# Performance work log

Measured on AMD Instinct MI355X. Metric: run time of the kernel, lower is better.

The kernel has to match this reference:

```python
import jax, jax.numpy as jnp
import numpy as np

B, T, D, H = 32, 512, 512, 512  # batch, seq_len, emb dim, lstm_size
TAGS = (17, 9, 25, 13)


def _reverse_sequence(x, lengths):
    # tf.reverse_sequence semantics: reverse first `len` steps, keep the tail.
    t = jnp.arange(x.shape[1])
    idx = jnp.where(t[None, :] < lengths[:, None], lengths[:, None] - 1 - t[None, :], t[None, :])
    return jnp.take_along_axis(x, idx[:, :, None], axis=1)


def _lstm(x, W, b, lengths):
    # TF LSTMCell: kernel [D+H,4H], gate order (i, j, f, o), forget_bias=1.0.
    # dynamic_rnn: state copied through past seq_len, outputs zeroed past seq_len.
    Bx, Tx, _ = x.shape
    Hh = b.shape[-1] // 4
    xT = jnp.swapaxes(x, 0, 1)  # [T,B,D]
    mask = (jnp.arange(Tx)[:, None] < lengths[None, :]).astype(x.dtype)[:, :, None]  # [T,B,1]

    def step(carry, inp):
        c, h = carry
        xt, m = inp
        z = jnp.concatenate([xt, h], axis=-1) @ W + b  # [B,4H]
        i, j, f, o = jnp.split(z, 4, axis=-1)
        c_new = jax.nn.sigmoid(f + 1.0) * c + jax.nn.sigmoid(i) * jnp.tanh(j)
        h_new = jax.nn.sigmoid(o) * jnp.tanh(c_new)
        c = m * c_new + (1.0 - m) * c
        h = m * h_new + (1.0 - m) * h
        return (c, h), h * m

    init = (jnp.zeros((Bx, Hh), x.dtype), jnp.zeros((Bx, Hh), x.dtype))
    _, hs = jax.lax.scan(step, init, (xT, mask))
    return jnp.swapaxes(hs, 0, 1)  # [B,T,H]


def _bilstm(x, lengths, Wf, bf, Wb, bb):
    out_fw = _lstm(x, Wf, bf, lengths)
    x_rev = _reverse_sequence(x, lengths)
    out_bw = _reverse_sequence(_lstm(x_rev, Wb, bb, lengths), lengths)
    return jnp.concatenate([out_fw, out_bw], axis=2)  # [B,T,2H]


def setup_inputs() -> dict:
    key = jax.random.key(0)
    ks = jax.random.split(key, 12)
    s_in = 1.0 / np.sqrt(D + H)
    s_fc = 1.0 / np.sqrt(4 * H)
    inp = {
        'embedded_words': jax.random.normal(ks[0], (B, T, D), jnp.float32),
        'sentence_lengths': jax.random.randint(ks[1], (B,), 16, T + 1, jnp.int32),
        'W_fw': jax.random.normal(ks[2], (5, D + H, 4 * H), jnp.float32) * s_in,
        'b_fw': jnp.zeros((5, 4 * H), jnp.float32),
        'W_bw': jax.random.normal(ks[3], (5, D + H, 4 * H), jnp.float32) * s_in,
        'b_bw': jnp.zeros((5, 4 * H), jnp.float32),
    }
    for i, tg in enumerate(TAGS):
        inp[f'W{i+1}'] = jax.random.normal(ks[4 + i], (4 * H, tg), jnp.float32) * s_fc
        inp[f'b{i+1}'] = jnp.zeros((tg,), jnp.float32)
    return inp


def reference(embedded_words, sentence_lengths, W_fw, b_fw, W_bw, b_bw,
              W1, b1, W2, b2, W3, b3, W4, b4):
    # 5 independent BiLSTMs (task1..4 + shared) over the same input, vmapped over the stack axis.
    outs = jax.vmap(lambda wf, bf, wb, bb: _bilstm(embedded_words, sentence_lengths, wf, bf, wb, bb))(
        W_fw, b_fw, W_bw, b_bw)  # [5,B,T,2H]
    shared = outs[4]
    logits = []
    for i, (Wk, bk) in enumerate(((W1, b1), (W2, b2), (W3, b3), (W4, b4))):
        feat = jnp.concatenate([outs[i], shared], axis=2)  # [B,T,4H]; dropout = identity (inference)
        logits.append(jnp.einsum('btd,dk->btk', feat, Wk) + bk)
    # concatenate the 4 task logit heads along the tag axis: [B,T,sum(TAGS)]
    return jnp.concatenate(logits, axis=2)
```

## Files before the change

### kernel.cpp

```cpp
#include <hip/hip_runtime.h>
#include <cstdint>
#include <cstddef>

#define BB 32
#define TT 512
#define DD 512
#define HH 512
#define FOURH 2048
#define DIRS 10
#define HSZ ((size_t)DIRS * BB * HH)
#define LWPITCH 520
#define SMEM_REC (128 * LWPITCH * 2 + 2 * 2 * 4 * 4 * 64 * 4)

typedef unsigned short u16;
typedef __attribute__((ext_vector_type(8))) short short8;
typedef __attribute__((ext_vector_type(4))) float f32x4;

__device__ __forceinline__ u16 f2b(float f) {
    union { float f; unsigned u; } v; v.f = f;
    unsigned u = v.u;
    u = (u + 0x7FFFu + ((u >> 16) & 1u)) >> 16;
    return (u16)u;
}
__device__ __forceinline__ float b2f(u16 b) {
    union { unsigned u; float f; } v; v.u = ((unsigned)b) << 16;
    return v.f;
}
__device__ __forceinline__ float sigm(float x) { return 1.f / (1.f + __expf(-x)); }
__device__ __forceinline__ float tanh_(float x) { return 1.f - 2.f / (1.f + __expf(2.f * x)); }
__device__ __forceinline__ f32x4 fzero() { f32x4 z = {0.f, 0.f, 0.f, 0.f}; return z; }

__device__ __forceinline__ uint4 load_coh16(const u16* p) {
    uint4 r;
    asm volatile("global_load_dwordx4 %0, %1, off sc0 sc1"
                 : "=v"(r) : "v"(p) : "memory");
    return r;
}

__global__ void k_convx(const float* __restrict__ X, u16* __restrict__ XB) {
    int i = blockIdx.x * 256 + threadIdx.x;
    if (i >= (BB * TT * DD) / 4) return;
    float4 v = ((const float4*)X)[i];
    unsigned lo = (unsigned)f2b(v.x) | ((unsigned)f2b(v.y) << 16);
    unsigned hi = (unsigned)f2b(v.z) | ((unsigned)f2b(v.w) << 16);
    uint2 o; o.x = lo; o.y = hi;
    ((uint2*)XB)[i] = o;
}

__global__ void k_wt(const float* __restrict__ Wf, const float* __restrict__ Wb,
                     u16* __restrict__ WT) {
    int d = blockIdx.z, s = d >> 1;
    const float* src = (d & 1) ? Wb : Wf;
    __shared__ float tile[32][33];
    int tx = threadIdx.x & 31, ty = threadIdx.x >> 5;
    int kt = blockIdx.x, nt = blockIdx.y;
#pragma unroll
    for (int r = 0; r < 4; r++) {
        int k = kt * 32 + ty + r * 8, n = nt * 32 + tx;
        tile[ty + r * 8][tx] = src[((size_t)s * 1024 + k) * 2048 + n];
    }
    __syncthreads();
#pragma unroll
    for (int r = 0; r < 4; r++) {
        int n = nt * 32 + ty + r * 8, k = kt * 32 + tx;
        WT[((size_t)d * 2048 + n) * 1024 + k] = f2b(tile[tx][ty + r * 8]);
    }
}

__global__ void k_wbt(const float* W1, const float* W2, const float* W3, const float* W4,
                      const float* b1, const float* b2, const float* b3, const float* b4,
                      u16* __restrict__ WBT, float* __restrict__ B64) {
    int idx = blockIdx.x * 256 + threadIdx.x;
    const int off[4] = {0, 17, 26, 51};
    const int tg[4]  = {17, 9, 25, 13};
    if (idx < 64) {
        int c = idx;
        int ti = (c < 17) ? 0 : (c < 26) ? 1 : (c < 51) ? 2 : 3;
        const float* bbp[4] = {b1, b2, b3, b4};
        B64[c] = bbp[ti][c - off[ti]];
    }
    if (idx >= 64 * 5120) return;
    int c = idx / 5120, k = idx % 5120;
    int ti = (c < 17) ? 0 : (c < 26) ? 1 : (c < 51) ? 2 : 3;
    const float* Ws[4] = {W1, W2, W3, W4};
    int tag = c - off[ti];
    float v;
    if (k < 4096) {
        int i = k >> 10, kk = k & 1023;
        v = (i == ti) ? Ws[ti][(size_t)kk * tg[ti] + tag] : 0.f;
    } else {
        int kk = k - 4096;
        v = Ws[ti][(size_t)(1024 + kk) * tg[ti] + tag];
    }
    WBT[(size_t)c * 5120 + k] = f2b(v);
}

__global__ __launch_bounds__(512, 2) void k_rec(
    const u16* __restrict__ WT, const u16* __restrict__ XB,
    const float* __restrict__ bfw, const float* __restrict__ bbw,
    u16* __restrict__ Hbuf, float* __restrict__ Cst, u16* __restrict__ OUTS,
    const int* __restrict__ lens, unsigned* __restrict__ ctr)
{
    extern __shared__ char smem[];
    u16* lWx = (u16*)smem;
    float* red = (float*)(smem + 128 * LWPITCH * 2);

    int blk = blockIdx.x, d = blk >> 4, jj = blk & 15;
    int s = d >> 1, isbw = d & 1;
    int tid = threadIdx.x, w = tid >> 6, lane = tid & 63, quad = lane >> 4, l15 = lane & 15;
    int mtile = w & 1, nhalf = (w >> 1) & 1, khalf = w >> 2;

#pragma unroll
    for (int it = 0; it < 16; ++it) {
        int g16 = it * 512 + tid;
        int row = g16 >> 6, c = g16 & 63;
        int n = (row >> 5) * 512 + jj * 32 + (row & 31);
        const u16* src = WT + ((size_t)d * 2048 + n) * 1024 + c * 8;
        *(uint4*)(lWx + row * LWPITCH + c * 8) = *(const uint4*)src;
    }

    short8 Bf[8][4];
#pragma unroll
    for (int ks = 0; ks < 8; ks++) {
        int k0 = khalf * 256 + ks * 32;
#pragma unroll
        for (int g = 0; g < 4; g++) {
            int n = g * 512 + jj * 32 + nhalf * 16 + l15;
            Bf[ks][g] = *(const short8*)(WT + ((size_t)d * 2048 + n) * 1024 + 512 + k0 + quad * 8);
        }
    }

    int bA = mtile * 16 + l15;
    int lbA = lens[bA];
    int ug = jj * 32 + nhalf * 16 + l15;
    const float* bias = (isbw ? bbw : bfw) + (size_t)s * 2048;
    float c_reg[4], hprev[4], bv_r[4];
    int lb_r[4];
    if (khalf == 0) {
#pragma unroll
        for (int g = 0; g < 4; g++) bv_r[g] = bias[g * 512 + ug];
#pragma unroll
        for (int r = 0; r < 4; r++) {
            int b = mtile * 16 + quad * 4 + r;
            lb_r[r] = lens[b];
            c_reg[r] = Cst[((size_t)d * BB + b) * HH + ug];
            hprev[r] = b2f(Hbuf[(size_t)d * BB * HH + (size_t)b * HH + ug]);
        }
    }
    __syncthreads();

    for (int t = 0; t < TT; ++t) {
        const u16* hin = Hbuf + (size_t)(t & 1) * HSZ + (size_t)d * BB * HH;
        u16* hout      = Hbuf + (size_t)((t + 1) & 1) * HSZ + (size_t)d * BB * HH;

        int srcT = isbw ? ((t < lbA) ? (lbA - 1 - t) : t) : t;
        const u16* xrow = XB + ((size_t)bA * TT + srcT) * DD + khalf * 256;
        uint4 xraw[8];
#pragma unroll
        for (int ks = 0; ks < 8; ks++)
            xraw[ks] = *(const uint4*)(xrow + ks * 32 + quad * 8);

        uint4 araw[8];
#pragma unroll
        for (int ks = 0; ks < 8; ks++)
            araw[ks] = load_coh16(hin + (size_t)bA * HH + khalf * 256 + ks * 32 + quad * 8);

        f32x4 acc[4];
#pragma unroll
        for (int g = 0; g < 4; g++) acc[g] = fzero();

#pragma unroll
        for (int ks = 0; ks < 8; ks++) {
            short8 a = *(const short8*)(&xraw[ks]);
#pragma unroll
            for (int g = 0; g < 4; g++) {
                short8 bfr = *(const short8*)(lWx + (g * 32 + nhalf * 16 + l15) * LWPITCH
                                              + khalf * 256 + ks * 32 + quad * 8);
                acc[g] = __builtin_amdgcn_mfma_f32_16x16x32_bf16(a, bfr, acc[g], 0, 0, 0);
            }
        }

        asm volatile("s_waitcnt vmcnt(0)" ::: "memory");
#pragma unroll
        for (int ks = 0; ks < 8; ks++) {
            short8 a = *(const short8*)(&araw[ks]);
#pragma unroll
            for (int g = 0; g < 4; g++)
                acc[g] = __builtin_amdgcn_mfma_f32_16x16x32_bf16(a, Bf[ks][g], acc[g], 0, 0, 0);
        }

        if (khalf == 1) {
#pragma unroll
            for (int g = 0; g < 4; g++)
#pragma unroll
                for (int r = 0; r < 4; r++)
                    red[((((size_t)mtile * 2 + nhalf) * 4 + g) * 4 + r) * 64 + lane] = acc[g][r];
        }
        __syncthreads();
        if (khalf == 0) {
#pragma unroll
            for (int g = 0; g < 4; g++)
#pragma unroll
                for (int r = 0; r < 4; r++)
                    acc[g][r] += red[((((size_t)mtile * 2 + nhalf) * 4 + g) * 4 + r) * 64 + lane];

#pragma unroll
            for (int r = 0; r < 4; r++) {
                int b = mtile * 16 + quad * 4 + r;
                int lb = lb_r[r];
                float zi = acc[0][r] + bv_r[0];
                float zj = acc[1][r] + bv_r[1];
                float zf = acc[2][r] + bv_r[2];
                float zo = acc[3][r] + bv_r[3];
                float cn = sigm(zf + 1.f) * c_reg[r] + sigm(zi) * tanh_(zj);
                float hn = sigm(zo) * tanh_(cn);
                bool act = t < lb;
                if (act) c_reg[r] = cn;
                u16 hv = f2b(act ? hn : hprev[r]);
                hprev[r] = b2f(hv);
                __hip_atomic_store(&hout[(size_t)b * HH + ug], hv,
                                   __ATOMIC_RELAXED, __HIP_MEMORY_SCOPE_AGENT);
                int twr = isbw ? (act ? (lb - 1 - t) : t) : t;
                OUTS[(((size_t)s * BB + b) * TT + twr) * 1024 + isbw * 512 + ug] = f2b(act ? hn : 0.f);
            }
        }

        __syncthreads();
        if (tid == 0) {
            atomicAdd(ctr + d * 16, 1u);
            unsigned target = 16u * (unsigned)(t + 1);
            while (__hip_atomic_load(ctr + d * 16, __ATOMIC_RELAXED, __HIP_MEMORY_SCOPE_AGENT) < target)
                __builtin_amdgcn_s_sleep(1);
        }
        __syncthreads();
    }
}

__global__ __launch_bounds__(256) void k_head(
    const u16* __restrict__ OUTS, const u16* __restrict__ WBT,
    const float* __restrict__ B64, float* __restrict__ OUT)
{
    int tid = threadIdx.x, w = tid >> 6, lane = tid & 63, quad = lane >> 4, l15 = lane & 15;
    int mtile = blockIdx.x * 4 + w, r0 = mtile * 16;
    int row_a = r0 + l15, ba = row_a >> 9, ta = row_a & 511;
    f32x4 acc[4];
#pragma unroll
    for (int ni = 0; ni < 4; ni++) acc[ni] = fzero();

    for (int k0 = 0; k0 < 5120; k0 += 32) {
        int kidx = k0 + quad * 8;
        int blkk = kidx >> 10, kk = kidx & 1023;
        short8 a = *(const short8*)(OUTS + (((size_t)blkk * BB + ba) * TT + ta) * 1024 + kk);
#pragma unroll
        for (int ni = 0; ni < 4; ni++) {
            short8 bf = *(const short8*)(WBT + (size_t)(ni * 16 + l15) * 5120 + kidx);
            acc[ni] = __builtin_amdgcn_mfma_f32_16x16x32_bf16(a, bf, acc[ni], 0, 0, 0);
        }
    }
#pragma unroll
    for (int ni = 0; ni < 4; ni++) {
        int c = ni * 16 + l15;
        float bv = B64[c];
#pragma unroll
        for (int r = 0; r < 4; r++) {
            int row = r0 + quad * 4 + r;
            OUT[(size_t)row * 64 + c] = acc[ni][r] + bv;
        }
    }
}

extern "C" void kernel_launch(void* const* d_in, const int* in_sizes, int n_in,
                              void* d_out, int out_size, void* d_ws, size_t ws_size,
                              hipStream_t stream) {
    const float* X   = (const float*)d_in[0];
    const int* lens  = (const int*)d_in[1];
    const float* Wf  = (const float*)d_in[2];
    const float* bf_ = (const float*)d_in[3];
    const float* Wb  = (const float*)d_in[4];
    const float* bb_ = (const float*)d_in[5];
    const float* W1  = (const float*)d_in[6];
    const float* b1  = (const float*)d_in[7];
    const float* W2  = (const float*)d_in[8];
    const float* b2  = (const float*)d_in[9];
    const float* W3  = (const float*)d_in[10];
    const float* b3  = (const float*)d_in[11];
    const float* W4  = (const float*)d_in[12];
    const float* b4  = (const float*)d_in[13];

    char* ws = (char*)d_ws;
    size_t off = 0;
    auto take = [&](size_t bytes) { size_t o = off; off += (bytes + 255) & ~(size_t)255; return o; };
    size_t wtOff   = take((size_t)DIRS * 2048 * 1024 * 2);
    size_t xbOff   = take((size_t)BB * TT * DD * 2);
    size_t outsOff = take((size_t)5 * BB * TT * 1024 * 2);
    size_t hOff    = take((size_t)2 * HSZ * 2);
    size_t cOff    = take((size_t)HSZ * 4);
    size_t ctrOff  = take((size_t)DIRS * 16 * 4);
    size_t wbtOff  = take((size_t)64 * 5120 * 2);
    size_t b64Off  = take((size_t)64 * 4);

    u16* WT    = (u16*)(ws + wtOff);
    u16* XB    = (u16*)(ws + xbOff);
    u16* OUTS  = (u16*)(ws + outsOff);
    u16* Hbuf  = (u16*)(ws + hOff);
    float* Cst = (float*)(ws + cOff);
    unsigned* CTR = (unsigned*)(ws + ctrOff);
    u16* WBT   = (u16*)(ws + wbtOff);
    float* B64 = (float*)(ws + b64Off);

    hipMemsetAsync(ws + hOff, 0, wbtOff - hOff, stream);

    (void)hipFuncSetAttribute((const void*)k_rec,
                              hipFuncAttributeMaxDynamicSharedMemorySize, SMEM_REC);

    k_convx<<<8192, 256, 0, stream>>>(X, XB);
    k_wt<<<dim3(32, 64, 10), 256, 0, stream>>>(Wf, Wb, WT);
    k_wbt<<<1280, 256, 0, stream>>>(W1, W2, W3, W4, b1, b2, b3, b4, WBT, B64);

    k_rec<<<160, 512, SMEM_REC, stream>>>(WT, XB, bf_, bb_, Hbuf, Cst, OUTS, lens, CTR);

    k_head<<<256, 256, 0, stream>>>(OUTS, WBT, B64, (float*)d_out);
}
```

Measured before the change: 3.692 ms.

## Replace counter barrier with per-block step flags and overlap wait with input MFMAs

```diff
diff --git a/kernel.cpp b/kernel.cpp
--- a/kernel.cpp
+++ b/kernel.cpp
@@ -6,7 +6,6 @@
 #define TT 512
 #define DD 512
 #define HH 512
-#define FOURH 2048
 #define DIRS 10
 #define HSZ ((size_t)DIRS * BB * HH)
 #define LWPITCH 520
@@ -98,8 +97,8 @@
 __global__ __launch_bounds__(512, 2) void k_rec(
     const u16* __restrict__ WT, const u16* __restrict__ XB,
     const float* __restrict__ bfw, const float* __restrict__ bbw,
-    u16* __restrict__ Hbuf, float* __restrict__ Cst, u16* __restrict__ OUTS,
-    const int* __restrict__ lens, unsigned* __restrict__ ctr)
+    u16* __restrict__ Hbuf, u16* __restrict__ OUTS,
+    const int* __restrict__ lens, unsigned* __restrict__ flg)
 {
     extern __shared__ char smem[];
     u16* lWx = (u16*)smem;
@@ -143,16 +142,14 @@
         for (int r = 0; r < 4; r++) {
             int b = mtile * 16 + quad * 4 + r;
             lb_r[r] = lens[b];
-            c_reg[r] = Cst[((size_t)d * BB + b) * HH + ug];
-            hprev[r] = b2f(Hbuf[(size_t)d * BB * HH + (size_t)b * HH + ug]);
-        }
-    }
+            c_reg[r] = 0.f;
+            hprev[r] = 0.f;
+        }
+    }
+    const unsigned* fline = flg + d * 16;
     __syncthreads();
 
     for (int t = 0; t < TT; ++t) {
-        const u16* hin = Hbuf + (size_t)(t & 1) * HSZ + (size_t)d * BB * HH;
-        u16* hout      = Hbuf + (size_t)((t + 1) & 1) * HSZ + (size_t)d * BB * HH;
-
         int srcT = isbw ? ((t < lbA) ? (lbA - 1 - t) : t) : t;
         const u16* xrow = XB + ((size_t)bA * TT + srcT) * DD + khalf * 256;
         uint4 xraw[8];
@@ -160,17 +157,12 @@
         for (int ks = 0; ks < 8; ks++)
             xraw[ks] = *(const uint4*)(xrow + ks * 32 + quad * 8);
 
-        uint4 araw[8];
-#pragma unroll
-        for (int ks = 0; ks < 8; ks++)
-            araw[ks] = load_coh16(hin + (size_t)bA * HH + khalf * 256 + ks * 32 + quad * 8);
-
         f32x4 acc[4];
 #pragma unroll
         for (int g = 0; g < 4; g++) acc[g] = fzero();
 
 #pragma unroll
-        for (int ks = 0; ks < 8; ks++) {
+        for (int ks = 0; ks < 6; ks++) {
             short8 a = *(const short8*)(&xraw[ks]);
 #pragma unroll
             for (int g = 0; g < 4; g++) {
@@ -180,7 +172,42 @@
             }
         }
 
+        {
+            unsigned tgt = (unsigned)t;
+            unsigned f = tgt;
+            if (lane < 16)
+                f = __hip_atomic_load(fline + lane, __ATOMIC_RELAXED,
+                                      __HIP_MEMORY_SCOPE_AGENT);
+            int spin = 0;
+            while (!__all((int)(f >= tgt)) && spin < (1 << 22)) {
+                __builtin_amdgcn_s_sleep(1);
+                f = tgt;
+                if (lane < 16)
+                    f = __hip_atomic_load(fline + lane, __ATOMIC_RELAXED,
+                                          __HIP_MEMORY_SCOPE_AGENT);
+                ++spin;
+            }
+        }
+
+        const u16* hin = Hbuf + (size_t)(t & 1) * HSZ + (size_t)d * BB * HH;
+        uint4 araw[8];
+#pragma unroll
+        for (int ks = 0; ks < 8; ks++)
+            araw[ks] = load_coh16(hin + (size_t)bA * HH + khalf * 256 + ks * 32 + quad * 8);
+
+#pragma unroll
+        for (int ks = 6; ks < 8; ks++) {
+            short8 a = *(const short8*)(&xraw[ks]);
+#pragma unroll
+            for (int g = 0; g < 4; g++) {
+                short8 bfr = *(const short8*)(lWx + (g * 32 + nhalf * 16 + l15) * LWPITCH
+                                              + khalf * 256 + ks * 32 + quad * 8);
+                acc[g] = __builtin_amdgcn_mfma_f32_16x16x32_bf16(a, bfr, acc[g], 0, 0, 0);
+            }
+        }
+
         asm volatile("s_waitcnt vmcnt(0)" ::: "memory");
+        __builtin_amdgcn_sched_barrier(0);
 #pragma unroll
         for (int ks = 0; ks < 8; ks++) {
             short8 a = *(const short8*)(&araw[ks]);
@@ -204,6 +231,7 @@
                 for (int r = 0; r < 4; r++)
                     acc[g][r] += red[((((size_t)mtile * 2 + nhalf) * 4 + g) * 4 + r) * 64 + lane];
 
+            u16* hout = Hbuf + (size_t)((t + 1) & 1) * HSZ + (size_t)d * BB * HH;
 #pragma unroll
             for (int r = 0; r < 4; r++) {
                 int b = mtile * 16 + quad * 4 + r;
@@ -224,15 +252,10 @@
                 OUTS[(((size_t)s * BB + b) * TT + twr) * 1024 + isbw * 512 + ug] = f2b(act ? hn : 0.f);
             }
         }
-
         __syncthreads();
-        if (tid == 0) {
-            atomicAdd(ctr + d * 16, 1u);
-            unsigned target = 16u * (unsigned)(t + 1);
-            while (__hip_atomic_load(ctr + d * 16, __ATOMIC_RELAXED, __HIP_MEMORY_SCOPE_AGENT) < target)
-                __builtin_amdgcn_s_sleep(1);
-        }
-        __syncthreads();
+        if (tid == 0)
+            __hip_atomic_store(flg + d * 16 + jj, (unsigned)(t + 1),
+                               __ATOMIC_RELAXED, __HIP_MEMORY_SCOPE_AGENT);
     }
 }
 
@@ -294,8 +317,7 @@
     size_t xbOff   = take((size_t)BB * TT * DD * 2);
     size_t outsOff = take((size_t)5 * BB * TT * 1024 * 2);
     size_t hOff    = take((size_t)2 * HSZ * 2);
-    size_t cOff    = take((size_t)HSZ * 4);
-    size_t ctrOff  = take((size_t)DIRS * 16 * 4);
+    size_t flgOff  = take((size_t)DIRS * 16 * 4);
     size_t wbtOff  = take((size_t)64 * 5120 * 2);
     size_t b64Off  = take((size_t)64 * 4);
 
@@ -303,8 +325,7 @@
     u16* XB    = (u16*)(ws + xbOff);
     u16* OUTS  = (u16*)(ws + outsOff);
     u16* Hbuf  = (u16*)(ws + hOff);
-    float* Cst = (float*)(ws + cOff);
-    unsigned* CTR = (unsigned*)(ws + ctrOff);
+    unsigned* FLG = (unsigned*)(ws + flgOff);
     u16* WBT   = (u16*)(ws + wbtOff);
     float* B64 = (float*)(ws + b64Off);
 
@@ -317,7 +338,7 @@
     k_wt<<<dim3(32, 64, 10), 256, 0, stream>>>(Wf, Wb, WT);
     k_wbt<<<1280, 256, 0, stream>>>(W1, W2, W3, W4, b1, b2, b3, b4, WBT, B64);
 
-    k_rec<<<160, 512, SMEM_REC, stream>>>(WT, XB, bf_, bb_, Hbuf, Cst, OUTS, lens, CTR);
+    k_rec<<<160, 512, SMEM_REC, stream>>>(WT, XB, bf_, bb_, Hbuf, OUTS, lens, FLG);
 
     k_head<<<256, 256, 0, stream>>>(OUTS, WBT, B64, (float*)d_out);
 }
```

New measurement: 3.125 ms. 15.4% less time.
